# Performance work log

Measured on AMD Instinct MI355X. Metric: run time of the kernel, lower is better.

## Reference

```python
import jax, jax.numpy as jnp
import numpy as np

B, S, D = 4, 2048, 1024

def _xavier(key, shape):
    bound = float(np.sqrt(6.0 / (shape[0] + shape[1])))
    return jax.random.uniform(key, shape, dtype=jnp.float32, minval=-bound, maxval=bound)

def setup_inputs() -> dict:
    key = jax.random.key(0)
    k0, k1, k2, k3 = jax.random.split(key, 4)
    return {
        "embeddings": jax.random.normal(k0, (B, S, D), dtype=jnp.float32),
        "W_Q": _xavier(k1, (D, D)),
        "W_K": _xavier(k2, (D, D)),
        "W_V": _xavier(k3, (D, D)),
    }

def reference(embeddings, W_Q, W_K, W_V):
    _, seq_len, d = embeddings.shape
    Q = embeddings @ W_Q                      # [B,S,D]
    K = embeddings @ W_K
    V = embeddings @ W_V
    scale = 1.0 / jnp.sqrt(jnp.float32(d))
    scores = jnp.einsum('bqd,bkd->bqk', Q, K) * scale   # [B,S,S]
    causal = jnp.tril(jnp.ones((seq_len, seq_len), dtype=bool))
    scores = jnp.where(causal[None, :, :], scores, -jnp.inf)
    probs = jax.nn.softmax(scores, axis=-1)
    return jnp.einsum('bqk,bkd->bqd', probs, V)
```

## Files before the change

kernel.cpp:

```cpp
#include <hip/hip_runtime.h>
#include <hip/hip_bf16.h>

#define BSZ 4
#define SEQ 2048
#define DIM 1024

typedef __attribute__((ext_vector_type(8))) short bf16x8;
typedef __attribute__((ext_vector_type(4))) float floatx4;

__device__ __forceinline__ unsigned short f2bf(float x) {
  union { float f; unsigned int u; } v; v.f = x;
  unsigned int r = v.u + 0x7fffu + ((v.u >> 16) & 1u);
  return (unsigned short)(r >> 16);
}

template <typename T> __device__ __forceinline__ void store_c(T* p, float v);
template <> __device__ __forceinline__ void store_c<float>(float* p, float v) { *p = v; }
template <> __device__ __forceinline__ void store_c<unsigned short>(unsigned short* p, float v) { *p = f2bf(v); }

__global__ __launch_bounds__(256) void prep(const float* __restrict__ E,
                                            const float* __restrict__ Wq,
                                            const float* __restrict__ Wk,
                                            const float* __restrict__ Wv,
                                            unsigned short* __restrict__ Ebf,
                                            unsigned short* __restrict__ WtQK,
                                            unsigned short* __restrict__ WtV,
                                            float* __restrict__ rsum, int n) {
  __shared__ float tile[32][33];
  int b = blockIdx.x;
  int tid = threadIdx.x;
  if (b < 8192) {
    if (b < 8) {
      int j = b * 1024 + tid * 4;
      *(float4*)(rsum + j) = make_float4(0.f, 0.f, 0.f, 0.f);
    }
    int i = (b * 256 + tid) * 4;
    if (i >= n) return;
    float4 v = *(const float4*)(E + i);
    ushort4 o;
    o.x = f2bf(v.x); o.y = f2bf(v.y); o.z = f2bf(v.z); o.w = f2bf(v.w);
    *(ushort4*)(Ebf + i) = o;
  } else {
    b -= 8192;
    int z = b >> 10;
    int rb = b & 1023;
    int bx = rb & 31, by = rb >> 5;
    const float* W = (z == 0) ? Wq : (z == 1) ? Wk : Wv;
    unsigned short* dst = (z == 2) ? WtV : WtQK;
    int row_off = (z == 1) ? 1024 : 0;
    int n0 = bx * 32, k0 = by * 32;
    int tx = tid & 31, ty = tid >> 5;
    for (int r = ty; r < 32; r += 8)
      tile[r][tx] = W[(size_t)(k0 + r) * DIM + n0 + tx];
    __syncthreads();
    for (int r = ty; r < 32; r += 8)
      dst[(size_t)(row_off + n0 + r) * DIM + k0 + tx] = f2bf(tile[tx][r]);
  }
}

__device__ __forceinline__ void gload16(const unsigned short* g, unsigned short* l) {
  __builtin_amdgcn_global_load_lds(
      (const __attribute__((address_space(1))) unsigned int*)g,
      (__attribute__((address_space(3))) unsigned int*)l, 16, 0, 0);
}

__device__ __forceinline__ void proj8ph(
    const unsigned short* __restrict__ A,
    const unsigned short* __restrict__ Bm,
    unsigned short* __restrict__ C, int ldc, int m0, int n0,
    unsigned short* sA, unsigned short* sB) {
  const int tid = threadIdx.x;
  const int lane = tid & 63;
  const int wid = tid >> 6;
  const int wm = (wid >> 2) * 128;
  const int wn = (wid & 3) * 64;
  const int lr = lane & 15, lq = lane >> 4;

  unsigned short* aB = sA + (wm >> 7) * 8192 + lr * 64;
  unsigned short* bB = sB + (wn >> 7) * 8192 + ((wn & 64) + lr) * 64;
  const int sw0 = (lq ^ (lr & 7)) * 8;
  const int sw1 = ((4 + lq) ^ (lr & 7)) * 8;

  const int schunk = (tid & 7) ^ ((tid >> 3) & 7);
  const unsigned short* gA = A + (size_t)(m0 + (tid >> 3)) * DIM + schunk * 8;
  const unsigned short* gB = Bm + (size_t)(n0 + (tid >> 3)) * DIM + schunk * 8;
  unsigned short* lA = sA + wid * 512;
  unsigned short* lB = sB + wid * 512;

#define STG_A(buf, T, half) do { \
    gload16(gA + (size_t)((half) * 128) * DIM + (T) * 64,      lA + (buf) * 16384 + (half) * 8192); \
    gload16(gA + (size_t)((half) * 128 + 64) * DIM + (T) * 64, lA + (buf) * 16384 + (half) * 8192 + 4096); } while (0)
#define STG_B(buf, T, half) do { \
    gload16(gB + (size_t)((half) * 128) * DIM + (T) * 64,      lB + (buf) * 16384 + (half) * 8192); \
    gload16(gB + (size_t)((half) * 128 + 64) * DIM + (T) * 64, lB + (buf) * 16384 + (half) * 8192 + 4096); } while (0)
#define RD_A(buf, qr) do { _Pragma("unroll") for (int i_ = 0; i_ < 4; ++i_) { \
    af[i_][0] = *(const bf16x8*)(aB + (buf) * 16384 + ((qr) * 64 + i_ * 16) * 64 + sw0); \
    af[i_][1] = *(const bf16x8*)(aB + (buf) * 16384 + ((qr) * 64 + i_ * 16) * 64 + sw1); } } while (0)
#define RD_B(buf, qc) do { _Pragma("unroll") for (int j_ = 0; j_ < 2; ++j_) { \
    bq[qc][j_][0] = *(const bf16x8*)(bB + (buf) * 16384 + ((qc) * 32 + j_ * 16) * 64 + sw0); \
    bq[qc][j_][1] = *(const bf16x8*)(bB + (buf) * 16384 + ((qc) * 32 + j_ * 16) * 64 + sw1); } } while (0)
#define MM(qr, qc) do { __builtin_amdgcn_s_setprio(1); \
    _Pragma("unroll") for (int i_ = 0; i_ < 4; ++i_) \
    _Pragma("unroll") for (int jj_ = 0; jj_ < 2; ++jj_) { \
      acc[(qr)*4+i_][(qc)*2+jj_] = __builtin_amdgcn_mfma_f32_16x16x32_bf16(af[i_][0], bq[qc][jj_][0], acc[(qr)*4+i_][(qc)*2+jj_], 0, 0, 0); \
      acc[(qr)*4+i_][(qc)*2+jj_] = __builtin_amdgcn_mfma_f32_16x16x32_bf16(af[i_][1], bq[qc][jj_][1], acc[(qr)*4+i_][(qc)*2+jj_], 0, 0, 0); } \
    __builtin_amdgcn_s_setprio(0); } while (0)
#define BAR __builtin_amdgcn_s_barrier()
#define LGKM0 do { asm volatile("s_waitcnt lgkmcnt(0)" ::: "memory"); __builtin_amdgcn_sched_barrier(0); } while (0)
#define VM4 asm volatile("s_waitcnt vmcnt(4)" ::: "memory")
#define VM0 asm volatile("s_waitcnt vmcnt(0)" ::: "memory")

  floatx4 acc[8][4] = {};
  bf16x8 af[4][2], bq[2][2][2];

  STG_B(0, 0, 0); STG_B(0, 0, 1);
  STG_A(0, 0, 0); STG_A(0, 0, 1);
  STG_B(1, 1, 0); STG_B(1, 1, 1);
  VM4;
  BAR;

#pragma unroll 1
  for (int j = 0; j < 8; ++j) {
    const int t0 = 2 * j, t1 = 2 * j + 1;
    const bool st = (j < 7);
    RD_A(0, 0); RD_B(0, 0);
    STG_A(1, t1, 0);
    BAR; LGKM0; MM(0, 0); BAR;

    RD_B(0, 1);
    STG_A(1, t1, 1);
    BAR; LGKM0; MM(0, 1); BAR;

    RD_A(0, 1);
    if (st) STG_B(0, t0 + 2, 0);
    BAR; LGKM0; MM(1, 0); BAR;

    if (st) STG_B(0, t0 + 2, 1);
    BAR; MM(1, 1);
    if (st) { VM4; } else { VM0; }
    BAR;

    RD_A(1, 0); RD_B(1, 0);
    if (st) STG_A(0, t0 + 2, 0);
    BAR; LGKM0; MM(0, 0); BAR;

    RD_B(1, 1);
    if (st) STG_A(0, t0 + 2, 1);
    BAR; LGKM0; MM(0, 1); BAR;

    RD_A(1, 1);
    if (st) STG_B(1, t1 + 2, 0);
    BAR; LGKM0; MM(1, 0); BAR;

    if (st) STG_B(1, t1 + 2, 1);
    BAR; MM(1, 1);
    if (st) { VM4; }
    BAR;
  }
#undef STG_A
#undef STG_B
#undef RD_A
#undef RD_B
#undef MM
#undef BAR
#undef LGKM0
#undef VM4
#undef VM0

#pragma unroll
  for (int i = 0; i < 8; ++i) {
    int rbase = m0 + wm + i * 16 + lq * 4;
#pragma unroll
    for (int jc = 0; jc < 4; ++jc) {
      int col = n0 + wn + jc * 16 + lr;
#pragma unroll
      for (int r = 0; r < 4; ++r)
        C[(size_t)(rbase + r) * ldc + col] = f2bf(acc[i][jc][r]);
    }
  }
}

#define NT_PROJ 32

template <int BMt>
__device__ __forceinline__ void proj_core(
    const unsigned short* __restrict__ A,
    const unsigned short* __restrict__ Bm,
    unsigned short* __restrict__ C, int ldc, int m0, int n0,
    unsigned short* sAr, unsigned short* sBr) {
  constexpr int LPA = BMt / 128;
  constexpr int LPT = LPA + 2;
  constexpr int FR  = BMt / 32;
  constexpr int TA  = BMt * 32;
  constexpr int TB  = 256 * 32;

  const int tid = threadIdx.x;
  const int lane = tid & 63;
  const int wid = tid >> 6;
  const int wm = (wid >> 2) * (BMt / 2);
  const int wn = (wid & 3) * 64;
  const int lr = lane & 15, lq = lane >> 4;

  const int srow = tid >> 2;
  const int schunk = (tid & 3) ^ ((tid >> 3) & 3);
  const unsigned short* gA = A + (size_t)(m0 + srow) * DIM + schunk * 8;
  const unsigned short* gB = Bm + (size_t)(n0 + srow) * DIM + schunk * 8;
  unsigned short* lA = sAr + 16 * 32 * wid;
  unsigned short* lB = sBr + 16 * 32 * wid;
  const size_t swG = (size_t)128 * DIM;

#define STAGE_A(T) do { int rb_ = (T) & 3; \
    gload16(gA + (size_t)(T) * 32, lA + rb_ * TA); \
    if constexpr (LPA == 2) gload16(gA + (size_t)(T) * 32 + swG, lA + rb_ * TA + 4096); } while (0)
#define STAGE_B(T) do { int rb_ = (T) & 3; \
    gload16(gB + (size_t)(T) * 32,       lB + rb_ * TB); \
    gload16(gB + (size_t)(T) * 32 + swG, lB + rb_ * TB + 4096); } while (0)
#define ARD(rb_, rowv) (*(const bf16x8*)&sAr[(rb_) * TA + (rowv) * 32 + (lq ^ (((rowv) >> 1) & 3)) * 8])
#define BRD(rb_, rowv) (*(const bf16x8*)&sBr[(rb_) * TB + (rowv) * 32 + (lq ^ (((rowv) >> 1) & 3)) * 8])

  floatx4 acc[FR][4] = {};

  STAGE_A(0); STAGE_B(0);
  STAGE_A(1); STAGE_B(1);
  STAGE_A(2); STAGE_B(2);
  if constexpr (LPT == 4) asm volatile("s_waitcnt vmcnt(8)" ::: "memory");
  else                    asm volatile("s_waitcnt vmcnt(6)" ::: "memory");
  __builtin_amdgcn_s_barrier();

#pragma unroll 4
  for (int T = 0; T < NT_PROJ; ++T) {
    const int rb = T & 3;
    bf16x8 af[4], bfr[4];
#pragma unroll
    for (int j = 0; j < 4; ++j) bfr[j] = BRD(rb, wn + j * 16 + lr);
#pragma unroll
    for (int i = 0; i < 4; ++i) af[i] = ARD(rb, wm + i * 16 + lr);
    if (T + 3 < NT_PROJ) {
      STAGE_A(T + 3);
      if constexpr (BMt == 128) STAGE_B(T + 3);
    }
    __builtin_amdgcn_s_barrier();
    __builtin_amdgcn_s_setprio(1);
#pragma unroll
    for (int i = 0; i < 4; ++i)
#pragma unroll
      for (int j = 0; j < 4; ++j)
        acc[i][j] = __builtin_amdgcn_mfma_f32_16x16x32_bf16(af[i], bfr[j], acc[i][j], 0, 0, 0);
    __builtin_amdgcn_s_setprio(0);
    if constexpr (BMt == 256) {
      __builtin_amdgcn_s_barrier();
#pragma unroll
      for (int i = 0; i < 4; ++i) af[i] = ARD(rb, wm + 64 + i * 16 + lr);
      if (T + 3 < NT_PROJ) STAGE_B(T + 3);
      __builtin_amdgcn_s_barrier();
      __builtin_amdgcn_s_setprio(1);
#pragma unroll
      for (int i = 0; i < 4; ++i)
#pragma unroll
        for (int j = 0; j < 4; ++j)
          acc[4 + i][j] = __builtin_amdgcn_mfma_f32_16x16x32_bf16(af[i], bfr[j], acc[4 + i][j], 0, 0, 0);
      __builtin_amdgcn_s_setprio(0);
    }
    if (T < NT_PROJ - 3) {
      if constexpr (LPT == 4) asm volatile("s_waitcnt vmcnt(8)" ::: "memory");
      else                    asm volatile("s_waitcnt vmcnt(6)" ::: "memory");
    } else if (T == NT_PROJ - 3) {
      if constexpr (LPT == 4) asm volatile("s_waitcnt vmcnt(4)" ::: "memory");
      else                    asm volatile("s_waitcnt vmcnt(3)" ::: "memory");
    } else if (T == NT_PROJ - 2) {
      asm volatile("s_waitcnt vmcnt(0)" ::: "memory");
    }
    __builtin_amdgcn_s_barrier();
  }
#undef STAGE_A
#undef STAGE_B
#undef ARD
#undef BRD

#pragma unroll
  for (int i = 0; i < FR; ++i) {
    int rbase = m0 + wm + i * 16 + lq * 4;
#pragma unroll
    for (int j = 0; j < 4; ++j) {
      int col = n0 + wn + j * 16 + lr;
#pragma unroll
      for (int r = 0; r < 4; ++r)
        C[(size_t)(rbase + r) * ldc + col] = f2bf(acc[i][j][r]);
    }
  }
}

__global__ __launch_bounds__(512, 2) void proj256(
    const unsigned short* __restrict__ Ebf,
    const unsigned short* __restrict__ WtQK,
    const unsigned short* __restrict__ WtV,
    unsigned short* __restrict__ QKo,
    unsigned short* __restrict__ Vt) {
  __shared__ __align__(16) unsigned short sA[32768];
  __shared__ __align__(16) unsigned short sB[32768];
  int x = blockIdx.x;
  if (x < 256) {
    proj8ph(Ebf, WtQK, QKo, 2 * DIM, (x >> 3) * 256, (x & 7) * 256, sA, sB);
  } else {
    x -= 256;
    proj_core<128>(WtV, Ebf, Vt, BSZ * SEQ, (x >> 5) * 128, (x & 31) * 256, sA, sB);
  }
}

template <typename OutT, int MODE>
__global__ __launch_bounds__(256, 2) void gemm_ring(
    const unsigned short* __restrict__ A, int lda, long long strideA,
    const unsigned short* __restrict__ B, int ldb, long long strideB,
    OutT* __restrict__ C, int ldc, long long strideC,
    int Kdim, float scale, float* __restrict__ rowsum) {
  int m0, n0;
  if constexpr (MODE == 1) {
    int t = blockIdx.x;
    int mt = 0;
    while (((mt + 1) * (mt + 2)) / 2 <= t) mt++;
    int nt = t - (mt * (mt + 1)) / 2;
    m0 = mt * 128; n0 = nt * 128;
  } else {
    int yy = ((blockIdx.z >> 1) & 1) ? blockIdx.y : (gridDim.y - 1 - blockIdx.y);
    m0 = yy * 128;
    n0 = blockIdx.x * 128;
  }
  const int Keff = (MODE == 2) ? min(Kdim, m0 + 128) : Kdim;
  const int NT = Keff >> 5;
  A += (long long)blockIdx.z * strideA;
  B += (long long)blockIdx.z * strideB;
  C += (long long)blockIdx.z * strideC;
  rowsum += (size_t)blockIdx.z * SEQ;

  __shared__ __align__(16) unsigned short sA[4 * 4096];
  __shared__ __align__(16) unsigned short sB[4 * 4096];

  const int tid = threadIdx.x;
  const int lane = tid & 63;
  const int wid = tid >> 6;
  const int wm = (wid >> 1) * 64, wn = (wid & 1) * 64;
  const int lr = lane & 15, lq = lane >> 4;

  const int schunk = (tid & 3) ^ ((tid >> 3) & 3);
  const unsigned short* gA = A + (size_t)(m0 + (tid >> 2)) * lda + schunk * 8;
  const unsigned short* gB = B + (size_t)(n0 + (tid >> 2)) * ldb + schunk * 8;
  unsigned short* lA = sA + wid * 512;
  unsigned short* lB = sB + wid * 512;
  const size_t sGA = (size_t)64 * lda, sGB = (size_t)64 * ldb;

#define RSTAGE(T) do { int rb_ = (T) & 3; \
    gload16(gA + (size_t)(T) * 32,       lA + rb_ * 4096); \
    gload16(gA + (size_t)(T) * 32 + sGA, lA + rb_ * 4096 + 2048); \
    gload16(gB + (size_t)(T) * 32,       lB + rb_ * 4096); \
    gload16(gB + (size_t)(T) * 32 + sGB, lB + rb_ * 4096 + 2048); } while (0)
#define RARD(rb_, rowv) (*(const bf16x8*)&sA[(rb_) * 4096 + (rowv) * 32 + (lq ^ (((rowv) >> 1) & 3)) * 8])
#define RBRD(rb_, rowv) (*(const bf16x8*)&sB[(rb_) * 4096 + (rowv) * 32 + (lq ^ (((rowv) >> 1) & 3)) * 8])

  floatx4 acc[4][4] = {};

  RSTAGE(0); RSTAGE(1); RSTAGE(2);
  asm volatile("s_waitcnt vmcnt(8)" ::: "memory");
  __builtin_amdgcn_s_barrier();

  for (int T = 0; T < NT; ++T) {
    const int rb = T & 3;
    bf16x8 af[4], bfr[4];
#pragma unroll
    for (int j = 0; j < 4; ++j) bfr[j] = RBRD(rb, wn + j * 16 + lr);
#pragma unroll
    for (int i = 0; i < 4; ++i) af[i] = RARD(rb, wm + i * 16 + lr);
    if (T + 3 < NT) RSTAGE(T + 3);
    __builtin_amdgcn_s_barrier();
    __builtin_amdgcn_s_setprio(1);
#pragma unroll
    for (int i = 0; i < 4; ++i)
#pragma unroll
      for (int j = 0; j < 4; ++j)
        acc[i][j] = __builtin_amdgcn_mfma_f32_16x16x32_bf16(af[i], bfr[j], acc[i][j], 0, 0, 0);
    __builtin_amdgcn_s_setprio(0);
    if (T < NT - 3)       asm volatile("s_waitcnt vmcnt(8)" ::: "memory");
    else if (T == NT - 3) asm volatile("s_waitcnt vmcnt(4)" ::: "memory");
    else if (T == NT - 2) asm volatile("s_waitcnt vmcnt(0)" ::: "memory");
    __builtin_amdgcn_s_barrier();
  }
#undef RSTAGE
#undef RARD
#undef RBRD

  if constexpr (MODE == 1) {
#pragma unroll
    for (int i = 0; i < 4; i++) {
      int rbase = m0 + wm + i * 16 + lq * 4;
      float s0 = 0.f, s1 = 0.f, s2 = 0.f, s3 = 0.f;
#pragma unroll
      for (int j = 0; j < 4; j++) {
        int col = n0 + wn + j * 16 + lr;
        float e0 = (col <= rbase + 0) ? __expf(acc[i][j][0] * scale) : 0.0f;
        float e1 = (col <= rbase + 1) ? __expf(acc[i][j][1] * scale) : 0.0f;
        float e2 = (col <= rbase + 2) ? __expf(acc[i][j][2] * scale) : 0.0f;
        float e3 = (col <= rbase + 3) ? __expf(acc[i][j][3] * scale) : 0.0f;
        store_c(&C[(size_t)(rbase + 0) * ldc + col], e0);
        store_c(&C[(size_t)(rbase + 1) * ldc + col], e1);
        store_c(&C[(size_t)(rbase + 2) * ldc + col], e2);
        store_c(&C[(size_t)(rbase + 3) * ldc + col], e3);
        s0 += e0; s1 += e1; s2 += e2; s3 += e3;
      }
#pragma unroll
      for (int m = 1; m < 16; m <<= 1) {
        s0 += __shfl_xor(s0, m, 64);
        s1 += __shfl_xor(s1, m, 64);
        s2 += __shfl_xor(s2, m, 64);
        s3 += __shfl_xor(s3, m, 64);
      }
      if (lr == 0) {
        atomicAdd(&rowsum[rbase + 0], s0);
        atomicAdd(&rowsum[rbase + 1], s1);
        atomicAdd(&rowsum[rbase + 2], s2);
        atomicAdd(&rowsum[rbase + 3], s3);
      }
    }
  } else {
#pragma unroll
    for (int i = 0; i < 4; i++) {
      int rbase = m0 + wm + i * 16 + lq * 4;
      float i0 = 1.0f / rowsum[rbase + 0];
      float i1 = 1.0f / rowsum[rbase + 1];
      float i2 = 1.0f / rowsum[rbase + 2];
      float i3 = 1.0f / rowsum[rbase + 3];
#pragma unroll
      for (int j = 0; j < 4; j++) {
        int col = n0 + wn + j * 16 + lr;
        store_c(&C[(size_t)(rbase + 0) * ldc + col], acc[i][j][0] * i0);
        store_c(&C[(size_t)(rbase + 1) * ldc + col], acc[i][j][1] * i1);
        store_c(&C[(size_t)(rbase + 2) * ldc + col], acc[i][j][2] * i2);
        store_c(&C[(size_t)(rbase + 3) * ldc + col], acc[i][j][3] * i3);
      }
    }
  }
}

extern "C" void kernel_launch(void* const* d_in, const int* in_sizes, int n_in,
                              void* d_out, int out_size, void* d_ws, size_t ws_size,
                              hipStream_t stream) {
  const float* E  = (const float*)d_in[0];
  const float* Wq = (const float*)d_in[1];
  const float* Wk = (const float*)d_in[2];
  const float* Wv = (const float*)d_in[3];
  float* out = (float*)d_out;

  char* ws = (char*)d_ws;
  size_t off = 0;
  auto alloc = [&](size_t bytes) {
    void* p = ws + off;
    off += (bytes + 255) & ~(size_t)255;
    return p;
  };
  const size_t M_ALL = (size_t)BSZ * SEQ;
  unsigned short* Ebf  = (unsigned short*)alloc(M_ALL * DIM * 2);
  unsigned short* WtQK = (unsigned short*)alloc((size_t)2 * DIM * DIM * 2);
  unsigned short* WtV  = (unsigned short*)alloc((size_t)DIM * DIM * 2);
  unsigned short* QK   = (unsigned short*)alloc(M_ALL * 2 * DIM * 2);
  unsigned short* Vt   = (unsigned short*)alloc((size_t)DIM * M_ALL * 2);
  unsigned short* ExpS = (unsigned short*)alloc((size_t)BSZ * SEQ * SEQ * 2);
  float*          Rsum = (float*)alloc((size_t)BSZ * SEQ * 4);

  int nE = (int)(M_ALL * DIM);
  prep<<<dim3(8192 + 3072), dim3(256), 0, stream>>>(E, Wq, Wk, Wv, Ebf, WtQK, WtV, Rsum, nE);

  proj256<<<dim3(512), dim3(512), 0, stream>>>(Ebf, WtQK, WtV, QK, Vt);

  gemm_ring<unsigned short, 1><<<dim3(136, 1, BSZ), dim3(256), 0, stream>>>(
      QK, 2 * DIM, (long long)SEQ * 2 * DIM,
      QK + DIM, 2 * DIM, (long long)SEQ * 2 * DIM,
      ExpS, SEQ, (long long)SEQ * SEQ,
      DIM, 0.03125f , Rsum);

  gemm_ring<float, 2><<<dim3(8, 16, BSZ), dim3(256), 0, stream>>>(
      ExpS, SEQ, (long long)SEQ * SEQ,
      Vt, (int)M_ALL, (long long)SEQ,
      out, DIM, (long long)SEQ * DIM,
      SEQ, 1.0f, Rsum);
}
```

Before: 234.8 us.

## Fold W_Q·W_Kᵀ into one matrix so scores use E·M against raw E

```diff
diff --git a/kernel.cpp b/kernel.cpp
--- a/kernel.cpp
+++ b/kernel.cpp
@@ -23,38 +23,43 @@
                                             const float* __restrict__ Wk,
                                             const float* __restrict__ Wv,
                                             unsigned short* __restrict__ Ebf,
-                                            unsigned short* __restrict__ WtQK,
+                                            unsigned short* __restrict__ Wqbf,
+                                            unsigned short* __restrict__ Wkbf,
                                             unsigned short* __restrict__ WtV,
-                                            float* __restrict__ rsum, int n) {
+                                            float* __restrict__ rsum) {
   __shared__ float tile[32][33];
   int b = blockIdx.x;
   int tid = threadIdx.x;
-  if (b < 8192) {
-    if (b < 8) {
-      int j = b * 1024 + tid * 4;
-      *(float4*)(rsum + j) = make_float4(0.f, 0.f, 0.f, 0.f);
-    }
-    int i = (b * 256 + tid) * 4;
-    if (i >= n) return;
-    float4 v = *(const float4*)(E + i);
+  if (b < 10240) {
+    const float* src;
+    unsigned short* dst;
+    int base;
+    if (b < 8192) {
+      if (b < 8) {
+        int j = b * 1024 + tid * 4;
+        *(float4*)(rsum + j) = make_float4(0.f, 0.f, 0.f, 0.f);
+      }
+      src = E; dst = Ebf; base = b;
+    } else if (b < 9216) {
+      src = Wq; dst = Wqbf; base = b - 8192;
+    } else {
+      src = Wk; dst = Wkbf; base = b - 9216;
+    }
+    int i = (base * 256 + tid) * 4;
+    float4 v = *(const float4*)(src + i);
     ushort4 o;
     o.x = f2bf(v.x); o.y = f2bf(v.y); o.z = f2bf(v.z); o.w = f2bf(v.w);
-    *(ushort4*)(Ebf + i) = o;
+    *(ushort4*)(dst + i) = o;
   } else {
-    b -= 8192;
-    int z = b >> 10;
-    int rb = b & 1023;
+    int rb = b - 10240;
     int bx = rb & 31, by = rb >> 5;
-    const float* W = (z == 0) ? Wq : (z == 1) ? Wk : Wv;
-    unsigned short* dst = (z == 2) ? WtV : WtQK;
-    int row_off = (z == 1) ? 1024 : 0;
     int n0 = bx * 32, k0 = by * 32;
     int tx = tid & 31, ty = tid >> 5;
     for (int r = ty; r < 32; r += 8)
-      tile[r][tx] = W[(size_t)(k0 + r) * DIM + n0 + tx];
+      tile[r][tx] = Wv[(size_t)(k0 + r) * DIM + n0 + tx];
     __syncthreads();
     for (int r = ty; r < 32; r += 8)
-      dst[(size_t)(row_off + n0 + r) * DIM + k0 + tx] = f2bf(tile[tx][r]);
+      WtV[(size_t)(n0 + r) * DIM + k0 + tx] = f2bf(tile[tx][r]);
   }
 }
 
@@ -62,122 +67,6 @@
   __builtin_amdgcn_global_load_lds(
       (const __attribute__((address_space(1))) unsigned int*)g,
       (__attribute__((address_space(3))) unsigned int*)l, 16, 0, 0);
-}
-
-__device__ __forceinline__ void proj8ph(
-    const unsigned short* __restrict__ A,
-    const unsigned short* __restrict__ Bm,
-    unsigned short* __restrict__ C, int ldc, int m0, int n0,
-    unsigned short* sA, unsigned short* sB) {
-  const int tid = threadIdx.x;
-  const int lane = tid & 63;
-  const int wid = tid >> 6;
-  const int wm = (wid >> 2) * 128;
-  const int wn = (wid & 3) * 64;
-  const int lr = lane & 15, lq = lane >> 4;
-
-  unsigned short* aB = sA + (wm >> 7) * 8192 + lr * 64;
-  unsigned short* bB = sB + (wn >> 7) * 8192 + ((wn & 64) + lr) * 64;
-  const int sw0 = (lq ^ (lr & 7)) * 8;
-  const int sw1 = ((4 + lq) ^ (lr & 7)) * 8;
-
-  const int schunk = (tid & 7) ^ ((tid >> 3) & 7);
-  const unsigned short* gA = A + (size_t)(m0 + (tid >> 3)) * DIM + schunk * 8;
-  const unsigned short* gB = Bm + (size_t)(n0 + (tid >> 3)) * DIM + schunk * 8;
-  unsigned short* lA = sA + wid * 512;
-  unsigned short* lB = sB + wid * 512;
-
-#define STG_A(buf, T, half) do { \
-    gload16(gA + (size_t)((half) * 128) * DIM + (T) * 64,      lA + (buf) * 16384 + (half) * 8192); \
-    gload16(gA + (size_t)((half) * 128 + 64) * DIM + (T) * 64, lA + (buf) * 16384 + (half) * 8192 + 4096); } while (0)
-#define STG_B(buf, T, half) do { \
-    gload16(gB + (size_t)((half) * 128) * DIM + (T) * 64,      lB + (buf) * 16384 + (half) * 8192); \
-    gload16(gB + (size_t)((half) * 128 + 64) * DIM + (T) * 64, lB + (buf) * 16384 + (half) * 8192 + 4096); } while (0)
-#define RD_A(buf, qr) do { _Pragma("unroll") for (int i_ = 0; i_ < 4; ++i_) { \
-    af[i_][0] = *(const bf16x8*)(aB + (buf) * 16384 + ((qr) * 64 + i_ * 16) * 64 + sw0); \
-    af[i_][1] = *(const bf16x8*)(aB + (buf) * 16384 + ((qr) * 64 + i_ * 16) * 64 + sw1); } } while (0)
-#define RD_B(buf, qc) do { _Pragma("unroll") for (int j_ = 0; j_ < 2; ++j_) { \
-    bq[qc][j_][0] = *(const bf16x8*)(bB + (buf) * 16384 + ((qc) * 32 + j_ * 16) * 64 + sw0); \
-    bq[qc][j_][1] = *(const bf16x8*)(bB + (buf) * 16384 + ((qc) * 32 + j_ * 16) * 64 + sw1); } } while (0)
-#define MM(qr, qc) do { __builtin_amdgcn_s_setprio(1); \
-    _Pragma("unroll") for (int i_ = 0; i_ < 4; ++i_) \
-    _Pragma("unroll") for (int jj_ = 0; jj_ < 2; ++jj_) { \
-      acc[(qr)*4+i_][(qc)*2+jj_] = __builtin_amdgcn_mfma_f32_16x16x32_bf16(af[i_][0], bq[qc][jj_][0], acc[(qr)*4+i_][(qc)*2+jj_], 0, 0, 0); \
-      acc[(qr)*4+i_][(qc)*2+jj_] = __builtin_amdgcn_mfma_f32_16x16x32_bf16(af[i_][1], bq[qc][jj_][1], acc[(qr)*4+i_][(qc)*2+jj_], 0, 0, 0); } \
-    __builtin_amdgcn_s_setprio(0); } while (0)
-#define BAR __builtin_amdgcn_s_barrier()
-#define LGKM0 do { asm volatile("s_waitcnt lgkmcnt(0)" ::: "memory"); __builtin_amdgcn_sched_barrier(0); } while (0)
-#define VM4 asm volatile("s_waitcnt vmcnt(4)" ::: "memory")
-#define VM0 asm volatile("s_waitcnt vmcnt(0)" ::: "memory")
-
-  floatx4 acc[8][4] = {};
-  bf16x8 af[4][2], bq[2][2][2];
-
-  STG_B(0, 0, 0); STG_B(0, 0, 1);
-  STG_A(0, 0, 0); STG_A(0, 0, 1);
-  STG_B(1, 1, 0); STG_B(1, 1, 1);
-  VM4;
-  BAR;
-
-#pragma unroll 1
-  for (int j = 0; j < 8; ++j) {
-    const int t0 = 2 * j, t1 = 2 * j + 1;
-    const bool st = (j < 7);
-    RD_A(0, 0); RD_B(0, 0);
-    STG_A(1, t1, 0);
-    BAR; LGKM0; MM(0, 0); BAR;
-
-    RD_B(0, 1);
-    STG_A(1, t1, 1);
-    BAR; LGKM0; MM(0, 1); BAR;
-
-    RD_A(0, 1);
-    if (st) STG_B(0, t0 + 2, 0);
-    BAR; LGKM0; MM(1, 0); BAR;
-
-    if (st) STG_B(0, t0 + 2, 1);
-    BAR; MM(1, 1);
-    if (st) { VM4; } else { VM0; }
-    BAR;
-
-    RD_A(1, 0); RD_B(1, 0);
-    if (st) STG_A(0, t0 + 2, 0);
-    BAR; LGKM0; MM(0, 0); BAR;
-
-    RD_B(1, 1);
-    if (st) STG_A(0, t0 + 2, 1);
-    BAR; LGKM0; MM(0, 1); BAR;
-
-    RD_A(1, 1);
-    if (st) STG_B(1, t1 + 2, 0);
-    BAR; LGKM0; MM(1, 0); BAR;
-
-    if (st) STG_B(1, t1 + 2, 1);
-    BAR; MM(1, 1);
-    if (st) { VM4; }
-    BAR;
-  }
-#undef STG_A
-#undef STG_B
-#undef RD_A
-#undef RD_B
-#undef MM
-#undef BAR
-#undef LGKM0
-#undef VM4
-#undef VM0
-
-#pragma unroll
-  for (int i = 0; i < 8; ++i) {
-    int rbase = m0 + wm + i * 16 + lq * 4;
-#pragma unroll
-    for (int jc = 0; jc < 4; ++jc) {
-      int col = n0 + wn + jc * 16 + lr;
-#pragma unroll
-      for (int r = 0; r < 4; ++r)
-        C[(size_t)(rbase + r) * ldc + col] = f2bf(acc[i][jc][r]);
-    }
-  }
 }
 
 #define NT_PROJ 32
@@ -290,21 +179,32 @@
   }
 }
 
-__global__ __launch_bounds__(512, 2) void proj256(
+__global__ __launch_bounds__(512, 2) void bulk1(
+    const unsigned short* __restrict__ Wkbf,
+    const unsigned short* __restrict__ Wqbf,
     const unsigned short* __restrict__ Ebf,
-    const unsigned short* __restrict__ WtQK,
     const unsigned short* __restrict__ WtV,
-    unsigned short* __restrict__ QKo,
+    unsigned short* __restrict__ Mt,
     unsigned short* __restrict__ Vt) {
-  __shared__ __align__(16) unsigned short sA[32768];
+  __shared__ __align__(16) unsigned short sA[16384];
   __shared__ __align__(16) unsigned short sB[32768];
   int x = blockIdx.x;
-  if (x < 256) {
-    proj8ph(Ebf, WtQK, QKo, 2 * DIM, (x >> 3) * 256, (x & 7) * 256, sA, sB);
+  if (x < 32) {
+    proj_core<128>(Wkbf, Wqbf, Mt, DIM, (x >> 2) * 128, (x & 3) * 256, sA, sB);
   } else {
-    x -= 256;
+    x -= 32;
     proj_core<128>(WtV, Ebf, Vt, BSZ * SEQ, (x >> 5) * 128, (x & 31) * 256, sA, sB);
   }
+}
+
+__global__ __launch_bounds__(512, 2) void bulk2(
+    const unsigned short* __restrict__ Ebf,
+    const unsigned short* __restrict__ Mt,
+    unsigned short* __restrict__ EM) {
+  __shared__ __align__(16) unsigned short sA[16384];
+  __shared__ __align__(16) unsigned short sB[32768];
+  int x = blockIdx.x;
+  proj_core<128>(Ebf, Mt, EM, DIM, (x >> 2) * 128, (x & 3) * 256, sA, sB);
 }
 
 template <typename OutT, int MODE>
@@ -457,21 +357,24 @@
   };
   const size_t M_ALL = (size_t)BSZ * SEQ;
   unsigned short* Ebf  = (unsigned short*)alloc(M_ALL * DIM * 2);
-  unsigned short* WtQK = (unsigned short*)alloc((size_t)2 * DIM * DIM * 2);
+  unsigned short* Wqbf = (unsigned short*)alloc((size_t)DIM * DIM * 2);
+  unsigned short* Wkbf = (unsigned short*)alloc((size_t)DIM * DIM * 2);
   unsigned short* WtV  = (unsigned short*)alloc((size_t)DIM * DIM * 2);
-  unsigned short* QK   = (unsigned short*)alloc(M_ALL * 2 * DIM * 2);
+  unsigned short* Mt   = (unsigned short*)alloc((size_t)DIM * DIM * 2);
+  unsigned short* EM   = (unsigned short*)alloc(M_ALL * DIM * 2);
   unsigned short* Vt   = (unsigned short*)alloc((size_t)DIM * M_ALL * 2);
   unsigned short* ExpS = (unsigned short*)alloc((size_t)BSZ * SEQ * SEQ * 2);
   float*          Rsum = (float*)alloc((size_t)BSZ * SEQ * 4);
 
-  int nE = (int)(M_ALL * DIM);
-  prep<<<dim3(8192 + 3072), dim3(256), 0, stream>>>(E, Wq, Wk, Wv, Ebf, WtQK, WtV, Rsum, nE);
-
-  proj256<<<dim3(512), dim3(512), 0, stream>>>(Ebf, WtQK, WtV, QK, Vt);
+  prep<<<dim3(11264), dim3(256), 0, stream>>>(E, Wq, Wk, Wv, Ebf, Wqbf, Wkbf, WtV, Rsum);
+
+  bulk1<<<dim3(288), dim3(512), 0, stream>>>(Wkbf, Wqbf, Ebf, WtV, Mt, Vt);
+
+  bulk2<<<dim3(256), dim3(512), 0, stream>>>(Ebf, Mt, EM);
 
   gemm_ring<unsigned short, 1><<<dim3(136, 1, BSZ), dim3(256), 0, stream>>>(
-      QK, 2 * DIM, (long long)SEQ * 2 * DIM,
-      QK + DIM, 2 * DIM, (long long)SEQ * 2 * DIM,
+      EM, DIM, (long long)SEQ * DIM,
+      Ebf, DIM, (long long)SEQ * DIM,
       ExpS, SEQ, (long long)SEQ * SEQ,
       DIM, 0.03125f , Rsum);
 
```

After: 241.0 us. 1.03x slower.

## Compute causal QK^T scores with 512-thread 128x256 tiled projection core

Applied to the files above, without the earlier changes.

```diff
diff --git a/kernel.cpp b/kernel.cpp
--- a/kernel.cpp
+++ b/kernel.cpp
@@ -182,12 +182,13 @@
 
 #define NT_PROJ 32
 
-template <int BMt>
+template <int BMt, int MODE = 0>
 __device__ __forceinline__ void proj_core(
-    const unsigned short* __restrict__ A,
-    const unsigned short* __restrict__ Bm,
+    const unsigned short* __restrict__ A, int lda,
+    const unsigned short* __restrict__ Bm, int ldb,
     unsigned short* __restrict__ C, int ldc, int m0, int n0,
-    unsigned short* sAr, unsigned short* sBr) {
+    unsigned short* sAr, unsigned short* sBr,
+    float scale = 0.f, float* __restrict__ rowsum = nullptr) {
   constexpr int LPA = BMt / 128;
   constexpr int LPT = LPA + 2;
   constexpr int FR  = BMt / 32;
@@ -203,18 +204,19 @@
 
   const int srow = tid >> 2;
   const int schunk = (tid & 3) ^ ((tid >> 3) & 3);
-  const unsigned short* gA = A + (size_t)(m0 + srow) * DIM + schunk * 8;
-  const unsigned short* gB = Bm + (size_t)(n0 + srow) * DIM + schunk * 8;
+  const unsigned short* gA = A + (size_t)(m0 + srow) * lda + schunk * 8;
+  const unsigned short* gB = Bm + (size_t)(n0 + srow) * ldb + schunk * 8;
   unsigned short* lA = sAr + 16 * 32 * wid;
   unsigned short* lB = sBr + 16 * 32 * wid;
-  const size_t swG = (size_t)128 * DIM;
+  const size_t swGA = (size_t)128 * lda;
+  const size_t swGB = (size_t)128 * ldb;
 
 #define STAGE_A(T) do { int rb_ = (T) & 3; \
     gload16(gA + (size_t)(T) * 32, lA + rb_ * TA); \
-    if constexpr (LPA == 2) gload16(gA + (size_t)(T) * 32 + swG, lA + rb_ * TA + 4096); } while (0)
+    if constexpr (LPA == 2) gload16(gA + (size_t)(T) * 32 + swGA, lA + rb_ * TA + 4096); } while (0)
 #define STAGE_B(T) do { int rb_ = (T) & 3; \
-    gload16(gB + (size_t)(T) * 32,       lB + rb_ * TB); \
-    gload16(gB + (size_t)(T) * 32 + swG, lB + rb_ * TB + 4096); } while (0)
+    gload16(gB + (size_t)(T) * 32,        lB + rb_ * TB); \
+    gload16(gB + (size_t)(T) * 32 + swGB, lB + rb_ * TB + 4096); } while (0)
 #define ARD(rb_, rowv) (*(const bf16x8*)&sAr[(rb_) * TA + (rowv) * 32 + (lq ^ (((rowv) >> 1) & 3)) * 8])
 #define BRD(rb_, rowv) (*(const bf16x8*)&sBr[(rb_) * TB + (rowv) * 32 + (lq ^ (((rowv) >> 1) & 3)) * 8])
 
@@ -277,15 +279,49 @@
 #undef ARD
 #undef BRD
 
-#pragma unroll
-  for (int i = 0; i < FR; ++i) {
-    int rbase = m0 + wm + i * 16 + lq * 4;
-#pragma unroll
-    for (int j = 0; j < 4; ++j) {
-      int col = n0 + wn + j * 16 + lr;
-#pragma unroll
-      for (int r = 0; r < 4; ++r)
-        C[(size_t)(rbase + r) * ldc + col] = f2bf(acc[i][j][r]);
+  if constexpr (MODE == 1) {
+#pragma unroll
+    for (int i = 0; i < FR; ++i) {
+      int rbase = m0 + wm + i * 16 + lq * 4;
+      float s0 = 0.f, s1 = 0.f, s2 = 0.f, s3 = 0.f;
+#pragma unroll
+      for (int j = 0; j < 4; ++j) {
+        int col = n0 + wn + j * 16 + lr;
+        float e0 = (col <= rbase + 0) ? __expf(acc[i][j][0] * scale) : 0.0f;
+        float e1 = (col <= rbase + 1) ? __expf(acc[i][j][1] * scale) : 0.0f;
+        float e2 = (col <= rbase + 2) ? __expf(acc[i][j][2] * scale) : 0.0f;
+        float e3 = (col <= rbase + 3) ? __expf(acc[i][j][3] * scale) : 0.0f;
+        C[(size_t)(rbase + 0) * ldc + col] = f2bf(e0);
+        C[(size_t)(rbase + 1) * ldc + col] = f2bf(e1);
+        C[(size_t)(rbase + 2) * ldc + col] = f2bf(e2);
+        C[(size_t)(rbase + 3) * ldc + col] = f2bf(e3);
+        s0 += e0; s1 += e1; s2 += e2; s3 += e3;
+      }
+#pragma unroll
+      for (int m = 1; m < 16; m <<= 1) {
+        s0 += __shfl_xor(s0, m, 64);
+        s1 += __shfl_xor(s1, m, 64);
+        s2 += __shfl_xor(s2, m, 64);
+        s3 += __shfl_xor(s3, m, 64);
+      }
+      if (lr == 0) {
+        atomicAdd(&rowsum[rbase + 0], s0);
+        atomicAdd(&rowsum[rbase + 1], s1);
+        atomicAdd(&rowsum[rbase + 2], s2);
+        atomicAdd(&rowsum[rbase + 3], s3);
+      }
+    }
+  } else {
+#pragma unroll
+    for (int i = 0; i < FR; ++i) {
+      int rbase = m0 + wm + i * 16 + lq * 4;
+#pragma unroll
+      for (int j = 0; j < 4; ++j) {
+        int col = n0 + wn + j * 16 + lr;
+#pragma unroll
+        for (int r = 0; r < 4; ++r)
+          C[(size_t)(rbase + r) * ldc + col] = f2bf(acc[i][j][r]);
+      }
     }
   }
 }
@@ -303,8 +339,25 @@
     proj8ph(Ebf, WtQK, QKo, 2 * DIM, (x >> 3) * 256, (x & 7) * 256, sA, sB);
   } else {
     x -= 256;
-    proj_core<128>(WtV, Ebf, Vt, BSZ * SEQ, (x >> 5) * 128, (x & 31) * 256, sA, sB);
-  }
+    proj_core<128>(WtV, DIM, Ebf, DIM, Vt, BSZ * SEQ, (x >> 5) * 128, (x & 31) * 256, sA, sB);
+  }
+}
+
+__global__ __launch_bounds__(512, 2) void scores512(
+    const unsigned short* __restrict__ QK,
+    unsigned short* __restrict__ ExpS,
+    float* __restrict__ Rsum) {
+  __shared__ __align__(16) unsigned short sA[16384];
+  __shared__ __align__(16) unsigned short sB[32768];
+  int t = blockIdx.x, mt = 0, s = 0;
+  while (s + (mt >> 1) + 1 <= t) { s += (mt >> 1) + 1; mt++; }
+  int nt = t - s;
+  const unsigned short* A = QK + (size_t)blockIdx.z * SEQ * 2 * DIM;
+  proj_core<128, 1>(A, 2 * DIM, A + DIM, 2 * DIM,
+                    ExpS + (size_t)blockIdx.z * SEQ * SEQ, SEQ,
+                    mt * 128, nt * 256, sA, sB,
+                    0.03125f ,
+                    Rsum + (size_t)blockIdx.z * SEQ);
 }
 
 template <typename OutT, int MODE>
@@ -465,15 +518,11 @@
   float*          Rsum = (float*)alloc((size_t)BSZ * SEQ * 4);
 
   int nE = (int)(M_ALL * DIM);
-  prep<<<dim3(8192 + 3072), dim3(256), 0, stream>>>(E, Wq, Wk, Wv, Ebf, WtQK, WtV, Rsum, nE);
+  prep<<<dim3(11264), dim3(256), 0, stream>>>(E, Wq, Wk, Wv, Ebf, WtQK, WtV, Rsum, nE);
 
   proj256<<<dim3(512), dim3(512), 0, stream>>>(Ebf, WtQK, WtV, QK, Vt);
 
-  gemm_ring<unsigned short, 1><<<dim3(136, 1, BSZ), dim3(256), 0, stream>>>(
-      QK, 2 * DIM, (long long)SEQ * 2 * DIM,
-      QK + DIM, 2 * DIM, (long long)SEQ * 2 * DIM,
-      ExpS, SEQ, (long long)SEQ * SEQ,
-      DIM, 0.03125f , Rsum);
+  scores512<<<dim3(72, 1, BSZ), dim3(512), 0, stream>>>(QK, ExpS, Rsum);
 
   gemm_ring<float, 2><<<dim3(8, 16, BSZ), dim3(256), 0, stream>>>(
       ExpS, SEQ, (long long)SEQ * SEQ,
```

Result: no change. 233.6 us (-0.5%).
